# Kernel optimization log

Hardware: AMD Instinct MI355X
Metric: run time of the kernel (lower is better)

## Reference

```python
import jax, jax.numpy as jnp
import numpy as np
import math

D = 1024
H = 16
NEG = -10000.0


def _layernorm(x, g, b, eps=1e-6):
    mu = x.mean(-1, keepdims=True)
    var = ((x - mu) ** 2).mean(-1, keepdims=True)
    return (x - mu) / jnp.sqrt(var + eps) * g + b


def _gelu(x):
    return x * 0.5 * (1.0 + jax.lax.erf(x / math.sqrt(2.0)))


def _split_heads(x):
    N, L, _ = x.shape
    return x.reshape(N, L, H, D // H).transpose(0, 2, 1, 3)  # (N,H,L,d)


def _attention(q, k, v, mask):
    # q,k,v: (N,Lq/Lk,D); mask: (N,1,Lq,Lk) of 0/1 or None
    d = D // H
    qh, kh, vh = _split_heads(q), _split_heads(k), _split_heads(v)
    scores = jnp.einsum('bhqd,bhkd->bhqk', qh, kh) / math.sqrt(d)
    if mask is not None:
        scores = scores + (1.0 - mask) * NEG
    probs = jax.nn.softmax(scores, axis=-1)
    ctx = jnp.einsum('bhqk,bhkd->bhqd', probs, vh)
    N, _, Lq, _ = ctx.shape
    ctx = ctx.transpose(0, 2, 1, 3).reshape(N, Lq, D)
    return ctx, scores.mean(1)  # attention_vis = masked scaled scores averaged over heads


def setup_inputs() -> dict:
    key = jax.random.key(0)
    ks = jax.random.split(key, 16)
    N, Lt, Lv = 16, 512, 512
    w = lambda k: (jax.random.normal(k, (D, D), jnp.float32) * 0.02)
    inp = {
        'dec_hidden_states': jax.random.normal(ks[0], (N, Lt, D), jnp.float32),
        'dec_mask': jnp.ones((N, Lt), jnp.float32),
        'enc_outputs': jax.random.normal(ks[1], (N, Lv, D), jnp.float32),
        'sa_wq': w(ks[2]), 'sa_bq': jnp.zeros((D,), jnp.float32),
        'sa_wk': w(ks[3]), 'sa_bk': jnp.zeros((D,), jnp.float32),
        'sa_wv': w(ks[4]), 'sa_bv': jnp.zeros((D,), jnp.float32),
        'n1_g': jnp.ones((D,), jnp.float32), 'n1_b': jnp.zeros((D,), jnp.float32),
        'ca_wq': w(ks[5]), 'ca_bq': jnp.zeros((D,), jnp.float32),
        'ca_wk': w(ks[6]), 'ca_bk': jnp.zeros((D,), jnp.float32),
        'ca_wv': w(ks[7]), 'ca_bv': jnp.zeros((D,), jnp.float32),
        'n2_g': jnp.ones((D,), jnp.float32), 'n2_b': jnp.zeros((D,), jnp.float32),
        'int_w': w(ks[8]), 'int_b': jnp.zeros((D,), jnp.float32),
        'out_w': w(ks[9]), 'out_b': jnp.zeros((D,), jnp.float32),
        'out_g': jnp.ones((D,), jnp.float32), 'out_beta': jnp.zeros((D,), jnp.float32),
    }
    return inp


def reference(dec_hidden_states, dec_mask, enc_outputs,
              sa_wq, sa_bq, sa_wk, sa_bk, sa_wv, sa_bv, n1_g, n1_b,
              ca_wq, ca_bq, ca_wk, ca_bk, ca_wv, ca_bv, n2_g, n2_b,
              int_w, int_b, out_w, out_b, out_g, out_beta):
    x = dec_hidden_states
    N, Lt, _ = x.shape
    # causal + padding mask: (N,1,Lt) * tril(Lt,Lt) -> (N,Lt,Lt) -> (N,1,Lt,Lt)
    causal = jnp.tril(jnp.ones((Lt, Lt), x.dtype))
    self_mask = (dec_mask[:, None, :] * causal)[:, None, :, :]
    # self attention
    q = x @ sa_wq + sa_bq
    k = x @ sa_wk + sa_bk
    v = x @ sa_wv + sa_bv
    sa_ctx, _ = _attention(q, k, v, self_mask)
    h = _layernorm(sa_ctx + x, n1_g, n1_b)
    # cross attention (no mask)
    cq = h @ ca_wq + ca_bq
    ck = enc_outputs @ ca_wk + ca_bk
    cv = enc_outputs @ ca_wv + ca_bv
    ca_ctx, attention_vis = _attention(cq, ck, cv, None)
    h2 = _layernorm(h + ca_ctx, n2_g, n2_b)
    # intermediate (gelu FFN)
    inter = _gelu(h2 @ int_w + int_b)
    # Output: dense + residual(intermediate itself, as in original) + LayerNorm
    out = _layernorm(inter @ out_w + out_b + inter, out_g, out_beta)
    return out, attention_vis
```

## Files before the change

### kernel.cpp

```cpp
#include <hip/hip_runtime.h>
#include <hip/hip_bf16.h>
#include <math.h>

#define DDIM 1024
#define NH   16
#define LTOK 512
#define NBATCH 16

typedef unsigned short u16;
typedef unsigned short u16x8 __attribute__((ext_vector_type(8)));
typedef unsigned short u16x4 __attribute__((ext_vector_type(4)));
typedef __bf16 bf16x8 __attribute__((ext_vector_type(8)));
typedef float f32x4 __attribute__((ext_vector_type(4)));

typedef __attribute__((address_space(1))) void as1_void;
typedef __attribute__((address_space(3))) void as3_void;

__device__ __forceinline__ void llds16(const u16* g, u16* l) {
    __builtin_amdgcn_global_load_lds((as1_void*)g, (as3_void*)l, 16, 0, 0);
}

__device__ __forceinline__ float bf2f(u16 u) {
    unsigned v = ((unsigned)u) << 16;
    float f; __builtin_memcpy(&f, &v, 4); return f;
}
__device__ __forceinline__ u16 f2bf(float f) {
    unsigned u; __builtin_memcpy(&u, &f, 4);
    u += 0x7fffu + ((u >> 16) & 1u);
    return (u16)(u >> 16);
}

struct GemmOp {
    const u16* A; const u16* B; u16* C; float* Cf; const float* bias;
    long sA1, sA2, sB1, sB2, sC1, sC2;
    int lda, ldb, ldc, M, N, K, zdiv, flags, nblk;
    float scale;
};

template<int MODE>
__global__ __launch_bounds__(256) void gemm_bt_kernel(GemmOp o1, GemmOp o2)
{
    constexpr int NB   = (MODE == 0) ? 1 : 2;
    constexpr int BUFE = 128 * 32;
    __shared__ __align__(16) u16 As[NB * BUFE];
    __shared__ __align__(16) u16 Bs[NB * BUFE];

    const bool second = (int)blockIdx.x >= o1.nblk;
    const GemmOp& o = second ? o2 : o1;
    int bidx = blockIdx.x - (second ? o1.nblk : 0);

    const int tilesN = o.N >> 7;
    const int tilesM = o.M >> 7;
    const int tiles  = tilesM * tilesN;
    const int z = bidx / tiles;
    const int t = bidx - z * tiles;
    const int zb = z / o.zdiv, zh = z - zb * o.zdiv;

    int tm, tn;
    if ((tilesM & 7) == 0) {
        const int xcd = t & 7, idx = t >> 3;
        const int mg  = tilesM >> 3;
        tm = ((idx % mg) << 3) | xcd;
        tn = idx / mg;
    } else {
        tm = t / tilesN;
        tn = t - tm * tilesN;
    }
    const int m0 = tm << 7, n0 = tn << 7;

    const u16* Ab = o.A + (long)zb * o.sA1 + (long)zh * o.sA2;
    const u16* Bb = o.B + (long)zb * o.sB1 + (long)zh * o.sB2;
    u16*   Cb  = o.C  ? o.C  + (long)zb * o.sC1 + (long)zh * o.sC2 : nullptr;
    float* Cfb = o.Cf ? o.Cf + (long)zb * o.sC1 + (long)zh * o.sC2 : nullptr;

    const int tid  = threadIdx.x;
    const int lane = tid & 63;
    const int wave = tid >> 6;
    const int wm = (wave & 1) << 6, wn = (wave >> 1) << 6;
    const int quad = lane >> 4, l16 = lane & 15;

    f32x4 acc[4][4];
#pragma unroll
    for (int i = 0; i < 4; i++)
#pragma unroll
        for (int j = 0; j < 4; j++) acc[i][j] = (f32x4){0.f, 0.f, 0.f, 0.f};

    const int lrA = (wave << 5) + (lane >> 2);
    const int lc  = (lane & 3) << 3;
    const u16* gA0 = Ab + (long)(m0 + lrA) * o.lda + lc;
    const u16* gA1 = Ab + (long)(m0 + lrA + 16) * o.lda + lc;
    const u16* gB0 = Bb + (long)(n0 + lrA) * o.ldb + lc;
    const u16* gB1 = Bb + (long)(n0 + lrA + 16) * o.ldb + lc;
    u16* lA0 = As + ((wave << 5) +  0) * 32;
    u16* lA1 = As + ((wave << 5) + 16) * 32;
    u16* lB0 = Bs + ((wave << 5) +  0) * 32;
    u16* lB1 = Bs + ((wave << 5) + 16) * 32;

    auto STAGE = [&](int bi, int k0) {
        llds16(gA0 + k0, lA0 + bi * BUFE);
        llds16(gA1 + k0, lA1 + bi * BUFE);
        llds16(gB0 + k0, lB0 + bi * BUFE);
        llds16(gB1 + k0, lB1 + bi * BUFE);
    };
    auto COMPUTE = [&](int bi) {
        const u16* Ac = As + bi * BUFE;
        const u16* Bc = Bs + bi * BUFE;
        bf16x8 af[4], bfr[4];
#pragma unroll
        for (int t2 = 0; t2 < 4; t2++)
            af[t2] = *(const bf16x8*)(Ac + (wm + t2 * 16 + l16) * 32 + quad * 8);
#pragma unroll
        for (int t2 = 0; t2 < 4; t2++)
            bfr[t2] = *(const bf16x8*)(Bc + (wn + t2 * 16 + l16) * 32 + quad * 8);
#pragma unroll
        for (int i = 0; i < 4; i++)
#pragma unroll
            for (int j = 0; j < 4; j++)
                acc[i][j] = __builtin_amdgcn_mfma_f32_16x16x32_bf16(
                    bfr[j], af[i], acc[i][j], 0, 0, 0);
    };

    const int K = o.K;
    if (MODE == 0) {
        for (int k0 = 0; k0 < K; k0 += 32) {
            __syncthreads();
            STAGE(0, k0);
            __syncthreads();
            COMPUTE(0);
        }
    } else {
        STAGE(0, 0);
        __syncthreads();
        int cur = 0;
        for (int k0 = 0; k0 < K; k0 += 32) {
            const int nxt = cur ^ 1;
            if (k0 + 32 < K) STAGE(nxt, k0 + 32);
            COMPUTE(cur);
            __syncthreads();
            cur = nxt;
        }
    }

#pragma unroll
    for (int i = 0; i < 4; i++) {
        const long row = m0 + wm + i * 16 + l16;
#pragma unroll
        for (int j = 0; j < 4; j++) {
            const int col = n0 + wn + j * 16 + quad * 4;
            f32x4 bv = o.bias ? *(const f32x4*)(o.bias + col)
                              : (f32x4){0.f, 0.f, 0.f, 0.f};
            f32x4 v4;
#pragma unroll
            for (int r = 0; r < 4; r++) {
                float v = acc[i][j][r] * o.scale + bv[r];
                if (o.flags & 1)
                    v = 0.5f * v * (1.f + erff(v * 0.70710678118654752f));
                v4[r] = v;
            }
            if (Cfb) {
                *(f32x4*)(Cfb + row * o.ldc + col) = v4;
            } else {
                u16x4 ov;
#pragma unroll
                for (int r = 0; r < 4; r++) ov[r] = f2bf(v4[r]);
                *(u16x4*)(Cb + row * o.ldc + col) = ov;
            }
        }
    }
}

__global__ __launch_bounds__(256, 4) void flash_kernel(
    const u16* __restrict__ Q, const u16* __restrict__ K,
    const u16* __restrict__ VT, u16* __restrict__ O,
    const float* __restrict__ mask, int causal, int ldq, int ldk)
{
    __shared__ __align__(16) u16 Ks[128 * 72];
    __shared__ __align__(16) u16 Vs[64 * 136];
    const int tid  = threadIdx.x;
    const int wave = tid >> 6, lane = tid & 63;
    const int quad = lane >> 4, l16 = lane & 15;
    const int bh = blockIdx.x, qt = blockIdx.y, b = bh >> 4, h = bh & 15;
    const int qbase = qt * 64 + wave * 16;
    const int qrow  = qbase + l16;

    const u16* qp = Q + ((long)b * LTOK + qrow) * ldq + h * 64 + quad * 8;
    bf16x8 aq0 = *(const bf16x8*)(qp);
    bf16x8 aq1 = *(const bf16x8*)(qp + 32);

    f32x4 oacc[4];
#pragma unroll
    for (int jd = 0; jd < 4; jd++) oacc[jd] = (f32x4){0.f, 0.f, 0.f, 0.f};
    float m_st = -3.0e38f;
    float l_st = 0.f;

    const int krow = tid >> 3,       kcol = (tid & 7) << 3;
    const int vrow = tid >> 2,       vcol = (tid & 3) << 3;
    const u16* gK = K + ((long)b * LTOK + krow) * ldk + h * 64 + kcol;
    const u16* gV = VT + ((long)bh * 64 + vrow) * LTOK + vcol;

    const float C1    = 0.125f * 1.44269504088896340736f;
    const float NEGL2 = -10000.0f * 1.44269504088896340736f;

    const int nkt = causal ? ((qt * 64 + 63) >> 7) + 1 : (LTOK >> 7);

    u16x8 KR[4], VR[4];
#pragma unroll
    for (int i = 0; i < 4; i++) KR[i] = *(const u16x8*)(gK + (long)(i * 32) * ldk);
#pragma unroll
    for (int i = 0; i < 4; i++) VR[i] = *(const u16x8*)(gV + i * 32);
#pragma unroll
    for (int i = 0; i < 4; i++)
        *(u16x8*)(Ks + (i * 32 + krow) * 72 + kcol) = KR[i];
#pragma unroll
    for (int i = 0; i < 4; i++)
        *(u16x8*)(Vs + vrow * 136 + i * 32 + vcol) = VR[i];
    __syncthreads();

    for (int kt = 0; kt < nkt; kt++) {
        const int k0 = kt << 7;
        const bool more = (kt + 1 < nkt);

        if (more) {
            const int kn = k0 + 128;
#pragma unroll
            for (int i = 0; i < 4; i++)
                KR[i] = *(const u16x8*)(gK + (long)(kn + i * 32) * ldk);
#pragma unroll
            for (int i = 0; i < 4; i++)
                VR[i] = *(const u16x8*)(gV + kn + i * 32);
        }

        f32x4 s[8];
#pragma unroll
        for (int j = 0; j < 8; j++) {
            bf16x8 bk0 = *(const bf16x8*)(Ks + (j * 16 + l16) * 72 + quad * 8);
            bf16x8 bk1 = *(const bf16x8*)(Ks + (j * 16 + l16) * 72 + 32 + quad * 8);
            f32x4 z = (f32x4){0.f, 0.f, 0.f, 0.f};
            z = __builtin_amdgcn_mfma_f32_16x16x32_bf16(bk0, aq0, z, 0, 0, 0);
            s[j] = __builtin_amdgcn_mfma_f32_16x16x32_bf16(bk1, aq1, z, 0, 0, 0);
        }

        float tm0 = -3.0e38f, tm1 = -3.0e38f, tm2 = -3.0e38f, tm3 = -3.0e38f;
#pragma unroll
        for (int j = 0; j < 8; j++) {
            if (causal) {
                f32x4 m4 = *(const f32x4*)(mask + (long)b * LTOK + k0 + j * 16 + quad * 4);
#pragma unroll
                for (int r = 0; r < 4; r++) {
                    int key = k0 + j * 16 + quad * 4 + r;
                    float ad = (key <= qrow) ? fmaf(m4[r], -NEGL2, NEGL2) : NEGL2;
                    s[j][r] = fmaf(s[j][r], C1, ad);
                }
            } else {
#pragma unroll
                for (int r = 0; r < 4; r++) s[j][r] *= C1;
            }
            tm0 = fmaxf(tm0, s[j][0]); tm1 = fmaxf(tm1, s[j][1]);
            tm2 = fmaxf(tm2, s[j][2]); tm3 = fmaxf(tm3, s[j][3]);
        }
        float tmax = fmaxf(fmaxf(tm0, tm1), fmaxf(tm2, tm3));
        tmax = fmaxf(tmax, __shfl_xor(tmax, 16));
        tmax = fmaxf(tmax, __shfl_xor(tmax, 32));

        float mnew  = fmaxf(m_st, tmax);
        float alpha = __builtin_amdgcn_exp2f(m_st - mnew);
        m_st = mnew;

        float rs0 = 0.f, rs1 = 0.f, rs2 = 0.f, rs3 = 0.f;
        unsigned pk[8][2];
#pragma unroll
        for (int j = 0; j < 8; j++) {
            float p0 = __builtin_amdgcn_exp2f(s[j][0] - mnew);
            float p1 = __builtin_amdgcn_exp2f(s[j][1] - mnew);
            float p2 = __builtin_amdgcn_exp2f(s[j][2] - mnew);
            float p3 = __builtin_amdgcn_exp2f(s[j][3] - mnew);
            rs0 += p0; rs1 += p1; rs2 += p2; rs3 += p3;
            asm("v_cvt_pk_bf16_f32 %0, %1, %2" : "=v"(pk[j][0]) : "v"(p0), "v"(p1));
            asm("v_cvt_pk_bf16_f32 %0, %1, %2" : "=v"(pk[j][1]) : "v"(p2), "v"(p3));
        }
        float rsum = (rs0 + rs1) + (rs2 + rs3);
        rsum += __shfl_xor(rsum, 16);
        rsum += __shfl_xor(rsum, 32);
        l_st = l_st * alpha + rsum;

#pragma unroll
        for (int jd = 0; jd < 4; jd++) oacc[jd] *= alpha;

#pragma unroll
        for (int kk = 0; kk < 4; kk++) {
            unsigned wv[4] = { pk[2 * kk][0], pk[2 * kk][1],
                               pk[2 * kk + 1][0], pk[2 * kk + 1][1] };
            bf16x8 bp; __builtin_memcpy(&bp, wv, 16);
#pragma unroll
            for (int jd = 0; jd < 4; jd++) {
                const u16* vb = Vs + (jd * 16 + l16) * 136 + kk * 32 + quad * 4;
                u16 va[8];
                *(u16x4*)(va)     = *(const u16x4*)(vb);
                *(u16x4*)(va + 4) = *(const u16x4*)(vb + 16);
                bf16x8 av; __builtin_memcpy(&av, va, 16);
                oacc[jd] = __builtin_amdgcn_mfma_f32_16x16x32_bf16(av, bp, oacc[jd], 0, 0, 0);
            }
        }

        if (more) {
            __syncthreads();
#pragma unroll
            for (int i = 0; i < 4; i++)
                *(u16x8*)(Ks + (i * 32 + krow) * 72 + kcol) = KR[i];
#pragma unroll
            for (int i = 0; i < 4; i++)
                *(u16x8*)(Vs + vrow * 136 + i * 32 + vcol) = VR[i];
            __syncthreads();
        }
    }

    float linv = 1.f / l_st;
    long obase = ((long)b * LTOK + qrow) * DDIM + h * 64;
#pragma unroll
    for (int jd = 0; jd < 4; jd++) {
        u16x4 ov;
#pragma unroll
        for (int r = 0; r < 4; r++) ov[r] = f2bf(oacc[jd][r] * linv);
        *(u16x4*)(O + obase + jd * 16 + quad * 4) = ov;
    }
}

__global__ __launch_bounds__(256) void add_ln_kernel(
    const u16* __restrict__ a, const u16* __restrict__ b,
    const float* __restrict__ b32,
    const float* __restrict__ g, const float* __restrict__ bt,
    u16* __restrict__ o, float* __restrict__ of)
{
    long row = blockIdx.x;
    int tid = threadIdx.x;
    __shared__ float red[4];
    const u16* ar = a + row * DDIM;
    float xv[4]; float s = 0.f;
#pragma unroll
    for (int i = 0; i < 4; i++) {
        int c = tid + 256 * i;
        float sum = bf2f(ar[c]) + (b32 ? b32[row * DDIM + c] : bf2f(b[row * DDIM + c]));
        xv[i] = fminf(fmaxf(sum, -1.0e18f), 1.0e18f);
        s += xv[i];
    }
#pragma unroll
    for (int ofs = 32; ofs >= 1; ofs >>= 1) s += __shfl_xor(s, ofs);
    int wave = tid >> 6, lane = tid & 63;
    if (lane == 0) red[wave] = s;
    __syncthreads();
    float mu = (red[0] + red[1] + red[2] + red[3]) * (1.f / 1024.f);
    __syncthreads();
    float v = 0.f;
#pragma unroll
    for (int i = 0; i < 4; i++) { float d = xv[i] - mu; v += d * d; }
#pragma unroll
    for (int ofs = 32; ofs >= 1; ofs >>= 1) v += __shfl_xor(v, ofs);
    if (lane == 0) red[wave] = v;
    __syncthreads();
    float var = (red[0] + red[1] + red[2] + red[3]) * (1.f / 1024.f);
    float inv = rsqrtf(var + 1e-6f);
#pragma unroll
    for (int i = 0; i < 4; i++) {
        int c = tid + 256 * i;
        float r = (xv[i] - mu) * inv * g[c] + bt[c];
        if (of) of[row * DDIM + c] = r;
        else    o [row * DDIM + c] = f2bf(r);
    }
}

__global__ __launch_bounds__(256) void cvt_kernel(
    const float* __restrict__ src, u16* __restrict__ dst)
{
    long i = ((long)blockIdx.x * 256 + threadIdx.x) * 8;
    u16x8 o;
#pragma unroll
    for (int j = 0; j < 8; j++) o[j] = f2bf(src[i + j]);
    *(u16x8*)(dst + i) = o;
}

__global__ __launch_bounds__(256) void wt_kernel(
    const float* w0, const float* w1, const float* w2, const float* w3,
    const float* w4, const float* w5, const float* w6, const float* w7,
    u16* __restrict__ wt)
{
    const float* srcs[8] = {w0, w1, w2, w3, w4, w5, w6, w7};
    const float* w = srcs[blockIdx.z];
    u16* o = wt + (long)blockIdx.z * DDIM * DDIM;
    __shared__ u16 t[32][33];
    int tx = threadIdx.x & 31, ty = threadIdx.x >> 5;
    int c0 = blockIdx.x << 5, r0 = blockIdx.y << 5;
#pragma unroll
    for (int i = 0; i < 4; i++)
        t[ty + 8 * i][tx] = f2bf(w[(long)(r0 + ty + 8 * i) * DDIM + c0 + tx]);
    __syncthreads();
#pragma unroll
    for (int i = 0; i < 4; i++)
        o[(long)(c0 + ty + 8 * i) * DDIM + r0 + tx] = t[tx][ty + 8 * i];
}

__global__ __launch_bounds__(256) void biascat_kernel(
    const float* __restrict__ b0, const float* __restrict__ b1,
    const float* __restrict__ b2, float* __restrict__ dst)
{
    int i = blockIdx.x * 256 + threadIdx.x;
    const float* s = (i < 1024) ? b0 : (i < 2048) ? b1 : b2;
    dst[i] = s[i & 1023];
}

__global__ __launch_bounds__(256) void vtrans_kernel(
    const u16* __restrict__ v, u16* __restrict__ vt, int ldv)
{
    int bh = blockIdx.y; int b = bh >> 4, h = bh & 15;
    int k0 = blockIdx.x << 5;
    __shared__ __align__(16) u16 t[32 * 72];
    int kk = threadIdx.x >> 3, c = (threadIdx.x & 7) << 3;
    u16x8 val = *(const u16x8*)(v + ((long)b * LTOK + k0 + kk) * ldv + h * 64 + c);
    *(u16x8*)(t + kk * 72 + c) = val;
    __syncthreads();
    int dd = threadIdx.x >> 2, k2 = (threadIdx.x & 3) << 3;
    u16x8 o;
#pragma unroll
    for (int j = 0; j < 8; j++) o[j] = t[(k2 + j) * 72 + dd];
    *(u16x8*)(vt + ((long)bh * 64 + dd) * LTOK + k0 + k2) = o;
}

extern "C" void kernel_launch(void* const* d_in, const int* in_sizes, int n_in,
                              void* d_out, int out_size, void* d_ws, size_t ws_size,
                              hipStream_t stream)
{
    const float* x     = (const float*)d_in[0];
    const float* dmsk  = (const float*)d_in[1];
    const float* enc   = (const float*)d_in[2];
    const float* sa_wq = (const float*)d_in[3];  const float* sa_bq = (const float*)d_in[4];
    const float* sa_wk = (const float*)d_in[5];  const float* sa_bk = (const float*)d_in[6];
    const float* sa_wv = (const float*)d_in[7];  const float* sa_bv = (const float*)d_in[8];
    const float* n1_g  = (const float*)d_in[9];  const float* n1_b  = (const float*)d_in[10];
    const float* ca_wq = (const float*)d_in[11]; const float* ca_bq = (const float*)d_in[12];
    const float* ca_wk = (const float*)d_in[13]; const float* ca_bk = (const float*)d_in[14];
    const float* ca_wv = (const float*)d_in[15]; const float* ca_bv = (const float*)d_in[16];
    const float* n2_g  = (const float*)d_in[17]; const float* n2_b  = (const float*)d_in[18];
    const float* int_w = (const float*)d_in[19]; const float* int_b = (const float*)d_in[20];
    const float* out_w = (const float*)d_in[21]; const float* out_b = (const float*)d_in[22];
    const float* out_g = (const float*)d_in[23]; const float* out_bt= (const float*)d_in[24];

    float* outp = (float*)d_out;
    float* visp = outp + (long)NBATCH * LTOK * DDIM;

    const size_t WTB  = (size_t)8 * DDIM * DDIM * 2;
    const size_t BUF1 = (size_t)LTOK * DDIM * 2;
    int cb = 16;
    while (cb > 1 && WTB + (size_t)cb * 7 * BUF1 + 32768 > ws_size)
        cb >>= 1;

    char* ws = (char*)d_ws;
    size_t off = 0;
    auto alloc = [&](size_t bytes) -> u16* {
        u16* p = (u16*)(ws + off);
        off += (bytes + 255) & ~(size_t)255;
        return p;
    };
    u16* Xb  = alloc((size_t)cb * BUF1);
    u16* Eb  = alloc((size_t)cb * BUF1);
    u16* Q3  = alloc((size_t)cb * 3 * BUF1);
    u16* Vt  = alloc((size_t)cb * BUF1);
    u16* Cx  = alloc((size_t)cb * BUF1);
    u16* WT  = alloc(WTB);
    float* biasQKV = (float*)alloc(3072 * sizeof(float));
    float* biasKV  = (float*)alloc(2048 * sizeof(float));

    u16* Wsaq = WT + 0L * DDIM * DDIM;
    u16* Wcaq = WT + 3L * DDIM * DDIM;
    u16* Wcak = WT + 4L * DDIM * DDIM;
    u16* Wint = WT + 6L * DDIM * DDIM;
    u16* Wout = WT + 7L * DDIM * DDIM;

    auto mkop = [](const u16* A, int lda, const u16* B, int ldb,
                   u16* C, float* Cf, int ldc, int M, int N, int K,
                   const float* bias, float scale, int flags) -> GemmOp {
        GemmOp o{};
        o.A = A; o.B = B; o.C = C; o.Cf = Cf; o.bias = bias;
        o.sA1 = 0; o.sA2 = 0; o.sB1 = 0; o.sB2 = 0; o.sC1 = 0; o.sC2 = 0;
        o.lda = lda; o.ldb = ldb; o.ldc = ldc; o.M = M; o.N = N; o.K = K;
        o.zdiv = 1; o.flags = flags; o.nblk = (M / 128) * (N / 128);
        o.scale = scale;
        return o;
    };

    auto launch = [&](GemmOp o1, GemmOp o2) {
        int nb = o1.nblk + o2.nblk;
        if (nb >= 1536)
            gemm_bt_kernel<0><<<dim3(nb), dim3(256), 0, stream>>>(o1, o2);
        else
            gemm_bt_kernel<1><<<dim3(nb), dim3(256), 0, stream>>>(o1, o2);
    };
    GemmOp nil{};

    const long SLD = (long)LTOK * DDIM;
    const long SSC = (long)LTOK * LTOK;

    wt_kernel<<<dim3(32, 32, 8), dim3(256), 0, stream>>>(
        sa_wq, sa_wk, sa_wv, ca_wq, ca_wk, ca_wv, int_w, out_w, WT);
    biascat_kernel<<<dim3(12), dim3(256), 0, stream>>>(sa_bq, sa_bk, sa_bv, biasQKV);
    biascat_kernel<<<dim3(8),  dim3(256), 0, stream>>>(ca_bk, ca_bv, ca_bv, biasKV);

    for (int b0 = 0; b0 < NBATCH; b0 += cb) {
        const float* xc = x   + (long)b0 * SLD;
        const float* ec = enc + (long)b0 * SLD;
        const int M = cb * LTOK;
        const int Z = cb * NH;
        const int cvtg = (int)(((long)M * DDIM) / (256 * 8));

        u16* h   = Xb;
        u16* CQ  = Q3;
        u16* CKV = Q3 + (size_t)cb * LTOK * DDIM;
        u16* I   = Vt;
        u16* G   = Cx;
        u16* h2  = Eb;

        cvt_kernel<<<dim3(cvtg), dim3(256), 0, stream>>>(xc, Xb);
        cvt_kernel<<<dim3(cvtg), dim3(256), 0, stream>>>(ec, Eb);

        launch(mkop(Xb, DDIM, Wsaq, DDIM, Q3, nullptr, 3 * DDIM,
                    M, 3 * DDIM, DDIM, biasQKV, 1.f, 0), nil);
        vtrans_kernel<<<dim3(16, Z), dim3(256), 0, stream>>>(Q3 + 2 * DDIM, Vt, 3 * DDIM);

        flash_kernel<<<dim3(Z, 8), dim3(256), 0, stream>>>(
            Q3, Q3 + DDIM, Vt, Cx, dmsk + (long)b0 * LTOK, 1, 3 * DDIM, 3 * DDIM);

        add_ln_kernel<<<dim3(M), dim3(256), 0, stream>>>(
            Cx, nullptr, xc, n1_g, n1_b, h, nullptr);

        launch(mkop(h,  DDIM, Wcaq, DDIM, CQ,  nullptr, DDIM,
                    M, DDIM, DDIM, ca_bq, 1.f, 0),
               mkop(Eb, DDIM, Wcak, DDIM, CKV, nullptr, 2 * DDIM,
                    M, 2 * DDIM, DDIM, biasKV, 1.f, 0));

        vtrans_kernel<<<dim3(16, Z), dim3(256), 0, stream>>>(CKV + DDIM, Vt, 2 * DDIM);
        flash_kernel<<<dim3(Z, 8), dim3(256), 0, stream>>>(
            CQ, CKV, Vt, Cx, nullptr, 0, DDIM, 2 * DDIM);

        add_ln_kernel<<<dim3(M), dim3(256), 0, stream>>>(
            h, Cx, nullptr, n2_g, n2_b, h2, nullptr);

        GemmOp ovis{};
        ovis.A = CQ;  ovis.lda = DDIM;     ovis.sA1 = SLD;               ovis.sA2 = 0;
        ovis.B = CKV; ovis.ldb = 2 * DDIM; ovis.sB1 = (long)LTOK * 2 * DDIM; ovis.sB2 = 0;
        ovis.C = nullptr; ovis.Cf = visp + (long)b0 * SSC;
        ovis.ldc = LTOK; ovis.sC1 = SSC; ovis.sC2 = 0;
        ovis.M = LTOK; ovis.N = LTOK; ovis.K = DDIM; ovis.zdiv = 1;
        ovis.bias = nullptr; ovis.scale = 1.f / 128.f; ovis.flags = 0;
        ovis.nblk = (LTOK / 128) * (LTOK / 128) * cb;
        launch(ovis,
               mkop(h2, DDIM, Wint, DDIM, I, nullptr, DDIM,
                    M, DDIM, DDIM, int_b, 1.f, 1));

        launch(mkop(I, DDIM, Wout, DDIM, G, nullptr, DDIM,
                    M, DDIM, DDIM, out_b, 1.f, 0), nil);

        add_ln_kernel<<<dim3(M), dim3(256), 0, stream>>>(
            G, I, nullptr, out_g, out_bt, nullptr, outp + (long)b0 * SLD);
    }
}
```

Before: 564.0 us.

## Fuse V transpose into GEMM epilogue and merge input conversion kernels

```diff
diff --git a/kernel.cpp b/kernel.cpp
--- a/kernel.cpp
+++ b/kernel.cpp
@@ -32,8 +32,9 @@
 
 struct GemmOp {
     const u16* A; const u16* B; u16* C; float* Cf; const float* bias;
+    u16* VTp;
     long sA1, sA2, sB1, sB2, sC1, sC2;
-    int lda, ldb, ldc, M, N, K, zdiv, flags, nblk;
+    int lda, ldb, ldc, M, N, K, zdiv, flags, nblk, vtcol0;
     float scale;
 };
 
@@ -157,7 +158,15 @@
                     v = 0.5f * v * (1.f + erff(v * 0.70710678118654752f));
                 v4[r] = v;
             }
-            if (Cfb) {
+            if (o.VTp && col >= o.vtcol0) {
+                const int dv  = col - o.vtcol0;
+                const long bh = (row >> 9) * NH + (dv >> 6);
+                const int tok = (int)(row & (LTOK - 1));
+                u16* vp = o.VTp + (bh * 64 + (dv & 63)) * LTOK + tok;
+#pragma unroll
+                for (int r = 0; r < 4; r++)
+                    vp[(long)r * LTOK] = f2bf(v4[r]);
+            } else if (Cfb) {
                 *(f32x4*)(Cfb + row * o.ldc + col) = v4;
             } else {
                 u16x4 ov;
@@ -368,9 +377,12 @@
     }
 }
 
-__global__ __launch_bounds__(256) void cvt_kernel(
-    const float* __restrict__ src, u16* __restrict__ dst)
-{
+__global__ __launch_bounds__(256) void cvt2_kernel(
+    const float* __restrict__ s0, u16* __restrict__ d0,
+    const float* __restrict__ s1, u16* __restrict__ d1)
+{
+    const float* src = blockIdx.y ? s1 : s0;
+    u16* dst = blockIdx.y ? d1 : d0;
     long i = ((long)blockIdx.x * 256 + threadIdx.x) * 8;
     u16x8 o;
 #pragma unroll
@@ -405,23 +417,6 @@
     int i = blockIdx.x * 256 + threadIdx.x;
     const float* s = (i < 1024) ? b0 : (i < 2048) ? b1 : b2;
     dst[i] = s[i & 1023];
-}
-
-__global__ __launch_bounds__(256) void vtrans_kernel(
-    const u16* __restrict__ v, u16* __restrict__ vt, int ldv)
-{
-    int bh = blockIdx.y; int b = bh >> 4, h = bh & 15;
-    int k0 = blockIdx.x << 5;
-    __shared__ __align__(16) u16 t[32 * 72];
-    int kk = threadIdx.x >> 3, c = (threadIdx.x & 7) << 3;
-    u16x8 val = *(const u16x8*)(v + ((long)b * LTOK + k0 + kk) * ldv + h * 64 + c);
-    *(u16x8*)(t + kk * 72 + c) = val;
-    __syncthreads();
-    int dd = threadIdx.x >> 2, k2 = (threadIdx.x & 3) << 3;
-    u16x8 o;
-#pragma unroll
-    for (int j = 0; j < 8; j++) o[j] = t[(k2 + j) * 72 + dd];
-    *(u16x8*)(vt + ((long)bh * 64 + dd) * LTOK + k0 + k2) = o;
 }
 
 extern "C" void kernel_launch(void* const* d_in, const int* in_sizes, int n_in,
@@ -479,6 +474,7 @@
                    const float* bias, float scale, int flags) -> GemmOp {
         GemmOp o{};
         o.A = A; o.B = B; o.C = C; o.Cf = Cf; o.bias = bias;
+        o.VTp = nullptr; o.vtcol0 = 0;
         o.sA1 = 0; o.sA2 = 0; o.sB1 = 0; o.sB2 = 0; o.sC1 = 0; o.sC2 = 0;
         o.lda = lda; o.ldb = ldb; o.ldc = ldc; o.M = M; o.N = N; o.K = K;
         o.zdiv = 1; o.flags = flags; o.nblk = (M / 128) * (N / 128);
@@ -486,9 +482,9 @@
         return o;
     };
 
-    auto launch = [&](GemmOp o1, GemmOp o2) {
+    auto launch = [&](int mode, GemmOp o1, GemmOp o2) {
         int nb = o1.nblk + o2.nblk;
-        if (nb >= 1536)
+        if (mode == 0)
             gemm_bt_kernel<0><<<dim3(nb), dim3(256), 0, stream>>>(o1, o2);
         else
             gemm_bt_kernel<1><<<dim3(nb), dim3(256), 0, stream>>>(o1, o2);
@@ -517,12 +513,14 @@
         u16* G   = Cx;
         u16* h2  = Eb;
 
-        cvt_kernel<<<dim3(cvtg), dim3(256), 0, stream>>>(xc, Xb);
-        cvt_kernel<<<dim3(cvtg), dim3(256), 0, stream>>>(ec, Eb);
-
-        launch(mkop(Xb, DDIM, Wsaq, DDIM, Q3, nullptr, 3 * DDIM,
-                    M, 3 * DDIM, DDIM, biasQKV, 1.f, 0), nil);
-        vtrans_kernel<<<dim3(16, Z), dim3(256), 0, stream>>>(Q3 + 2 * DDIM, Vt, 3 * DDIM);
+        cvt2_kernel<<<dim3(cvtg, 2), dim3(256), 0, stream>>>(xc, Xb, ec, Eb);
+
+        {
+            GemmOp o = mkop(Xb, DDIM, Wsaq, DDIM, Q3, nullptr, 3 * DDIM,
+                            M, 3 * DDIM, DDIM, biasQKV, 1.f, 0);
+            o.VTp = Vt; o.vtcol0 = 2 * DDIM;
+            launch(0, o, nil);
+        }
 
         flash_kernel<<<dim3(Z, 8), dim3(256), 0, stream>>>(
             Q3, Q3 + DDIM, Vt, Cx, dmsk + (long)b0 * LTOK, 1, 3 * DDIM, 3 * DDIM);
@@ -530,12 +528,14 @@
         add_ln_kernel<<<dim3(M), dim3(256), 0, stream>>>(
             Cx, nullptr, xc, n1_g, n1_b, h, nullptr);
 
-        launch(mkop(h,  DDIM, Wcaq, DDIM, CQ,  nullptr, DDIM,
-                    M, DDIM, DDIM, ca_bq, 1.f, 0),
-               mkop(Eb, DDIM, Wcak, DDIM, CKV, nullptr, 2 * DDIM,
-                    M, 2 * DDIM, DDIM, biasKV, 1.f, 0));
-
-        vtrans_kernel<<<dim3(16, Z), dim3(256), 0, stream>>>(CKV + DDIM, Vt, 2 * DDIM);
+        {
+            GemmOp okv = mkop(Eb, DDIM, Wcak, DDIM, CKV, nullptr, 2 * DDIM,
+                              M, 2 * DDIM, DDIM, biasKV, 1.f, 0);
+            okv.VTp = Vt; okv.vtcol0 = DDIM;
+            launch(1, mkop(h, DDIM, Wcaq, DDIM, CQ, nullptr, DDIM,
+                           M, DDIM, DDIM, ca_bq, 1.f, 0), okv);
+        }
+
         flash_kernel<<<dim3(Z, 8), dim3(256), 0, stream>>>(
             CQ, CKV, Vt, Cx, nullptr, 0, DDIM, 2 * DDIM);
 
@@ -546,16 +546,17 @@
         ovis.A = CQ;  ovis.lda = DDIM;     ovis.sA1 = SLD;               ovis.sA2 = 0;
         ovis.B = CKV; ovis.ldb = 2 * DDIM; ovis.sB1 = (long)LTOK * 2 * DDIM; ovis.sB2 = 0;
         ovis.C = nullptr; ovis.Cf = visp + (long)b0 * SSC;
+        ovis.VTp = nullptr; ovis.vtcol0 = 0;
         ovis.ldc = LTOK; ovis.sC1 = SSC; ovis.sC2 = 0;
         ovis.M = LTOK; ovis.N = LTOK; ovis.K = DDIM; ovis.zdiv = 1;
         ovis.bias = nullptr; ovis.scale = 1.f / 128.f; ovis.flags = 0;
         ovis.nblk = (LTOK / 128) * (LTOK / 128) * cb;
-        launch(ovis,
+        launch(1, ovis,
                mkop(h2, DDIM, Wint, DDIM, I, nullptr, DDIM,
                     M, DDIM, DDIM, int_b, 1.f, 1));
 
-        launch(mkop(I, DDIM, Wout, DDIM, G, nullptr, DDIM,
-                    M, DDIM, DDIM, out_b, 1.f, 0), nil);
+        launch(1, mkop(I, DDIM, Wout, DDIM, G, nullptr, DDIM,
+                       M, DDIM, DDIM, out_b, 1.f, 0), nil);
 
         add_ln_kernel<<<dim3(M), dim3(256), 0, stream>>>(
             G, I, nullptr, out_g, out_bt, nullptr, outp + (long)b0 * SLD);
```

Result: faster. 548.8 us (-2.7%).
